# Kernel tuning notes

Measured on AMD Instinct MI355X. Metric: run time of the kernel, lower is better.

## Reference

```python
import jax, jax.numpy as jnp
import numpy as np

B, L, C, H, W = 1, 16, 16, 128, 256  # L = T_chunk = K_chunk (single chunk, causal)
DECAY = 0.1  # decay_val


def setup_inputs() -> dict:
    key = jax.random.key(0)
    k1, k2 = jax.random.split(key)
    img = jax.random.normal(k1, (B, L, C, H, W), jnp.float32)
    # flows in normalized [-1,1] grid units; keep displacements modest
    cum_flow = jax.random.normal(k2, (B, L, 2, H, W), jnp.float32) * 0.1
    t = jnp.arange(L)
    mask = (t[:, None] >= t[None, :]).astype(jnp.float32)          # causal [T,K]
    decay_dist = jnp.abs(t[:, None] - t[None, :]).astype(jnp.float32)  # [T,K]
    return {"img": img, "cum_flow": cum_flow, "mask": mask, "decay_dist": decay_dist}


def _bilinear_sample(img, gx, gy):
    # img: [B,K,C,H,W]; gx, gy: [B,K,H,W] in normalized [-1,1] coords.
    # x wraps around (periodic), y clamps -- matching the kernel's index handling.
    ix = (gx + 1.0) * (W * 0.5) - 0.5
    iy = (gy + 1.0) * (H * 0.5) - 0.5
    x0 = jnp.floor(ix)
    y0 = jnp.floor(iy)
    wx = ix - x0  # fractional weights
    wy = iy - y0
    x0i = x0.astype(jnp.int32)
    y0i = y0.astype(jnp.int32)
    x0r = jnp.mod(x0i, W)
    x1r = jnpp = jnp.mod(x0i + 1, W)
    y0c = jnp.clip(y0i, 0, H - 1)
    y1c = jnp.clip(y0i + 1, 0, H - 1)

    K = img.shape[1]
    imgf = img.reshape(B, K, C, H * W)

    def gather(yy, xx):
        idx = (yy * W + xx).reshape(B, K, 1, H * W)  # broadcast over C
        return jnp.take_along_axis(imgf, idx, axis=-1).reshape(B, K, C, H, W)

    va = gather(y0c, x0r)  # (y0, x0)
    vb = gather(y1c, x0r)  # (y1, x0)
    vc = gather(y0c, x1r)  # (y0, x1)
    vd = gather(y1c, x1r)  # (y1, x1)
    wx_ = wx[:, :, None]   # [B,K,1,H,W]
    wy_ = wy[:, :, None]
    return (va * (1.0 - wx_) * (1.0 - wy_) + vb * (1.0 - wx_) * wy_
            + vc * wx_ * (1.0 - wy_) + vd * wx_ * wy_)


def reference(img, cum_flow, mask, decay_dist):
    # base grid (align_corners=False style pixel centers)
    base_x = (jnp.arange(W, dtype=jnp.float32) * (2.0 / W) - 1.0 + 1.0 / W)[None, None, :]  # [1,1,W]
    base_y = (jnp.arange(H, dtype=jnp.float32) * (2.0 / H) - 1.0 + 1.0 / H)[None, :, None]  # [1,H,1]

    weights = mask * jnp.exp(-DECAY * decay_dist)  # [T,K] decay-weighted causal mask
    fx = cum_flow[:, :, 0]  # [B,L,H,W]
    fy = cum_flow[:, :, 1]

    def step(carry, inp):
        ft_x, ft_y, w_row = inp  # ft_*: [B,H,W]; w_row: [K]
        gx = base_x[None] + (ft_x[:, None] - fx)  # [B,K,H,W]
        gy = base_y[None] + (ft_y[:, None] - fy)
        gx = jnp.mod(gx + 1.0, 2.0) - 1.0          # wrap x into [-1,1)
        sampled = _bilinear_sample(img, gx, gy)    # [B,K,C,H,W]
        out_t = jnp.einsum('k,bkchw->bchw', w_row, sampled)
        return carry, out_t

    xs = (jnp.moveaxis(fx, 1, 0), jnp.moveaxis(fy, 1, 0), weights)  # over t
    _, outs = jax.lax.scan(step, 0.0, xs)          # [T,B,C,H,W]
    return jnp.moveaxis(outs, 0, 1)                # [B,T,C,H,W]
```

## Files before the change

### kernel.cpp

```cpp
#include <hip/hip_runtime.h>

constexpr int Lc = 16;
constexpr int Cc = 16;
constexpr int Hc = 128;
constexpr int Wc = 256;
constexpr float DECAYc = 0.1f;
constexpr int HWc = Hc * Wc;

__device__ inline unsigned short f2bf(float f) {
    unsigned int u = __float_as_uint(f);
    u += 0x7fffu + ((u >> 16) & 1u);
    return (unsigned short)(u >> 16);
}
__device__ inline float2 bf2f2(unsigned int u) {
    return make_float2(__uint_as_float(u << 16),
                       __uint_as_float(u & 0xffff0000u));
}

constexpr int topbit(unsigned m) { int r = 0; while (m >>= 1) ++r; return r; }

__global__ __launch_bounds__(256) void transpose_cvt_bf16(
    const float* __restrict__ img, unsigned short* __restrict__ imgTb)
{
    const int tid = threadIdx.x;
    const int h2 = tid & 1;
    const int wq = tid >> 1;
    const int kf  = blockIdx.x >> 5;
    const int px0 = (blockIdx.x & 31) * 1024;
    const float* __restrict__ srcb = img + (size_t)kf * Cc * HWc + (size_t)(8 * h2) * HWc;
#pragma unroll
    for (int rr = 0; rr < 8; ++rr) {
        const int px = px0 + rr * 128 + wq;
        float v[8];
#pragma unroll
        for (int c = 0; c < 8; ++c) v[c] = srcb[c * HWc + px];
        uint4 o;
        o.x = (unsigned int)f2bf(v[0]) | ((unsigned int)f2bf(v[1]) << 16);
        o.y = (unsigned int)f2bf(v[2]) | ((unsigned int)f2bf(v[3]) << 16);
        o.z = (unsigned int)f2bf(v[4]) | ((unsigned int)f2bf(v[5]) << 16);
        o.w = (unsigned int)f2bf(v[6]) | ((unsigned int)f2bf(v[7]) << 16);
        *(uint4*)(imgTb + ((size_t)kf * HWc + px) * Cc + 8 * h2) = o;
    }
}

template <unsigned MASK, int TLO, int THI>
__device__ __forceinline__ void do_chunk16(
    int k, const unsigned short* __restrict__ bk, int half,
    const float* sx1, const float* sy1, float fxk, float fyk,
    const float* __restrict__ wtab, float (*acc)[8])
{
    constexpr int NT = THI - TLO + 1;
    int   offs[NT][4];
    float wts [NT][4];
    uint4 ld  [NT][4];

#pragma unroll
    for (int t = TLO; t <= THI; ++t) {
        if (!((MASK >> t) & 1u)) continue;
        if (t > k) {
            const int j = t - TLO;
            const float wkt = wtab[t * Lc + k];
            const float ix = (sx1[t] - fxk) * (Wc * 0.5f) - 0.5f;
            const float iy = (sy1[t] - fyk) * (Hc * 0.5f) - 0.5f;
            const float x0f = floorf(ix);
            const float y0f = floorf(iy);
            const float wx = ix - x0f;
            const float wy = iy - y0f;
            const int x0 = (int)x0f;
            const int y0 = (int)y0f;
            const int x0r = x0 & (Wc - 1);
            const int x1r = (x0 + 1) & (Wc - 1);
            const int y0c = min(max(y0, 0), Hc - 1);
            const int y1c = min(max(y0 + 1, 0), Hc - 1);
            const float wb = wkt * wy;
            const float wa = wkt - wb;
            const float omx = 1.0f - wx;
            wts[j][0] = wa * omx;
            wts[j][1] = wa * wx;
            wts[j][2] = wb * omx;
            wts[j][3] = wb * wx;
            offs[j][0] = y0c * Wc + x0r;
            offs[j][1] = y0c * Wc + x1r;
            offs[j][2] = y1c * Wc + x0r;
            offs[j][3] = y1c * Wc + x1r;
        }
    }
#pragma unroll
    for (int t = TLO; t <= THI; ++t) {
        if (!((MASK >> t) & 1u)) continue;
        if (t > k) {
            const int j = t - TLO;
#pragma unroll
            for (int n = 0; n < 4; ++n)
                ld[j][n] = ((const uint4*)(bk + (size_t)offs[j][n] * Cc))[half];
        }
    }
#pragma unroll
    for (int t = TLO; t <= THI; ++t) {
        if (!((MASK >> t) & 1u)) continue;
        if (t > k) {
            const int j = t - TLO;
#pragma unroll
            for (int n = 0; n < 4; ++n) {
                const float a = wts[j][n];
                const float2 f01 = bf2f2(ld[j][n].x);
                const float2 f23 = bf2f2(ld[j][n].y);
                const float2 f45 = bf2f2(ld[j][n].z);
                const float2 f67 = bf2f2(ld[j][n].w);
                acc[t][0] += a * f01.x;
                acc[t][1] += a * f01.y;
                acc[t][2] += a * f23.x;
                acc[t][3] += a * f23.y;
                acc[t][4] += a * f45.x;
                acc[t][5] += a * f45.y;
                acc[t][6] += a * f67.x;
                acc[t][7] += a * f67.y;
            }
        }
    }
}

template <unsigned MASK>
__device__ __forceinline__ void run_quarter(
    const unsigned short* __restrict__ imgTb,
    const float* __restrict__ cum_flow,
    const float* __restrict__ img,
    float* __restrict__ out,
    const float* wtab,
    int half, int pix, float base_x, float base_y)
{
    constexpr unsigned LOOPM = MASK & ~1u;

    float sx1[Lc], sy1[Lc];
#pragma unroll
    for (int t = 0; t < Lc; ++t) {
        if (!((LOOPM >> t) & 1u)) continue;
        sx1[t] = base_x + cum_flow[(t * 2 + 0) * HWc + pix] + 1.0f;
        sy1[t] = base_y + cum_flow[(t * 2 + 1) * HWc + pix] + 1.0f;
    }

    float acc[Lc][8];
#pragma unroll
    for (int t = 0; t < Lc; ++t) {
        if (!((MASK >> t) & 1u)) continue;
#pragma unroll
        for (int c = 0; c < 8; ++c) acc[t][c] = 0.f;
    }

    constexpr int KMAX = topbit(MASK);
    for (int k = 0; k < KMAX; ++k) {
        const float fxk = cum_flow[(k * 2 + 0) * HWc + pix];
        const float fyk = cum_flow[(k * 2 + 1) * HWc + pix];
        const unsigned short* __restrict__ bk = imgTb + (size_t)k * HWc * Cc;
        do_chunk16<LOOPM, 1, 7>(k, bk, half, sx1, sy1, fxk, fyk, wtab, acc);
        do_chunk16<LOOPM, 8, 15>(k, bk, half, sx1, sy1, fxk, fyk, wtab, acc);
    }

#pragma unroll
    for (int t = 0; t < Lc; ++t) {
        if (!((MASK >> t) & 1u)) continue;
        const float* __restrict__ ip = img + ((size_t)t * Cc + 8 * half) * HWc + pix;
        float* __restrict__ op = out + ((size_t)t * Cc + 8 * half) * HWc + pix;
#pragma unroll
        for (int c = 0; c < 8; ++c)
            op[c * HWc] = acc[t][c] + ip[c * HWc];
    }
}

__global__ __launch_bounds__(256, 4) void gridsample_bf16_h16(
    const unsigned short* __restrict__ imgTb,
    const float* __restrict__ cum_flow,
    const float* __restrict__ mask,
    const float* __restrict__ decay,
    const float* __restrict__ img,
    float* __restrict__ out)
{
    __shared__ float wtab[Lc * Lc];
    const int tid = threadIdx.x;
    if (tid < Lc * Lc)
        wtab[tid] = mask[tid] * __expf(-DECAYc * decay[tid]);
    __syncthreads();

    const int half = tid & 1;
    const int px32 = (tid >> 1) & 31;
    const int wv   = tid >> 6;
    const int b    = blockIdx.x;
    const int band = b & 7;
    const int sub  = b >> 3;
    const int h = band * 16 + (sub >> 3);
    const int w = (sub & 7) * 32 + px32;
    const int pix = h * Wc + w;

    const float base_x = w * (2.0f / Wc) - 1.0f + 1.0f / Wc;
    const float base_y = h * (2.0f / Hc) - 1.0f + 1.0f / Hc;

    switch (wv) {
        case 0:  run_quarter<0x8124u>(imgTb, cum_flow, img, out, wtab, half, pix, base_x, base_y); break;
        case 1:  run_quarter<0x4242u>(imgTb, cum_flow, img, out, wtab, half, pix, base_x, base_y); break;
        case 2:  run_quarter<0x2418u>(imgTb, cum_flow, img, out, wtab, half, pix, base_x, base_y); break;
        default: run_quarter<0x1881u>(imgTb, cum_flow, img, out, wtab, half, pix, base_x, base_y); break;
    }
}

__global__ __launch_bounds__(256) void gridsample_warp_acc(
    const float* __restrict__ img, const float* __restrict__ cum_flow,
    const float* __restrict__ mask, const float* __restrict__ decay,
    float* __restrict__ out)
{
    const int w = threadIdx.x, h = blockIdx.x, t = blockIdx.y;
    const int pix = h * Wc + w;
    const float base_x = w * (2.0f / Wc) - 1.0f + 1.0f / Wc;
    const float base_y = h * (2.0f / Hc) - 1.0f + 1.0f / Hc;
    const float fxt = cum_flow[(t * 2 + 0) * HWc + pix];
    const float fyt = cum_flow[(t * 2 + 1) * HWc + pix];
    float acc[Cc];
#pragma unroll
    for (int c = 0; c < Cc; ++c) acc[c] = 0.0f;
    for (int k = 0; k <= t; ++k) {
        const float wkt = mask[t * Lc + k] * __expf(-DECAYc * decay[t * Lc + k]);
        const float fxk = cum_flow[(k * 2 + 0) * HWc + pix];
        const float fyk = cum_flow[(k * 2 + 1) * HWc + pix];
        float gx = base_x + (fxt - fxk);
        const float gy = base_y + (fyt - fyk);
        float m = gx + 1.0f;
        m -= 2.0f * floorf(m * 0.5f);
        gx = m - 1.0f;
        const float ix = (gx + 1.0f) * (Wc * 0.5f) - 0.5f;
        const float iy = (gy + 1.0f) * (Hc * 0.5f) - 0.5f;
        const float x0f = floorf(ix), y0f = floorf(iy);
        const float wx = ix - x0f, wy = iy - y0f;
        const int x0 = (int)x0f, y0 = (int)y0f;
        const int x0r = x0 & (Wc - 1), x1r = (x0 + 1) & (Wc - 1);
        const int y0c = min(max(y0, 0), Hc - 1), y1c = min(max(y0 + 1, 0), Hc - 1);
        const float a00 = wkt * (1.0f - wx) * (1.0f - wy);
        const float a01 = wkt * (1.0f - wx) * wy;
        const float a10 = wkt * wx * (1.0f - wy);
        const float a11 = wkt * wx * wy;
        const int o00 = y0c * Wc + x0r, o01 = y1c * Wc + x0r;
        const int o10 = y0c * Wc + x1r, o11 = y1c * Wc + x1r;
        const float* __restrict__ ik = img + (size_t)k * Cc * HWc;
#pragma unroll
        for (int c = 0; c < Cc; ++c) {
            const float* __restrict__ p = ik + c * HWc;
            acc[c] += p[o00] * a00 + p[o01] * a01 + p[o10] * a10 + p[o11] * a11;
        }
    }
    float* __restrict__ op = out + (size_t)t * Cc * HWc + pix;
#pragma unroll
    for (int c = 0; c < Cc; ++c) op[c * HWc] = acc[c];
}

extern "C" void kernel_launch(void* const* d_in, const int* in_sizes, int n_in,
                              void* d_out, int out_size, void* d_ws, size_t ws_size,
                              hipStream_t stream) {
    const float* img      = (const float*)d_in[0];
    const float* cum_flow = (const float*)d_in[1];
    const float* mask     = (const float*)d_in[2];
    const float* decay    = (const float*)d_in[3];
    float* out = (float*)d_out;

    const size_t needed = (size_t)Lc * HWc * Cc * sizeof(unsigned short);
    if (ws_size >= needed) {
        unsigned short* imgTb = (unsigned short*)d_ws;
        transpose_cvt_bf16<<<dim3(512), 256, 0, stream>>>(img, imgTb);
        gridsample_bf16_h16<<<dim3(1024), 256, 0, stream>>>(
            imgTb, cum_flow, mask, decay, img, out);
    } else {
        dim3 grid(Hc, Lc, 1);
        gridsample_warp_acc<<<grid, Wc, 0, stream>>>(img, cum_flow, mask, decay, out);
    }
}
```

Baseline: 162.6 us.

## Split channel halves across blocks so each wave covers 64 contiguous pixels

Before, the two 8-channel halves of a pixel sat in adjacent lanes of a wave, so each wave covered 32 pixels. Now the channel half is chosen per block (the top bit of the block index), and each wave handles 64 consecutive pixels of one half. Per-pixel flow loads and output stores become fully coalesced 64-wide accesses with no lane pairs sharing a pixel. The cost is that each bilinear gather now reads 16 bytes at a 32-byte stride, and each wave recomputes offsets and weights for twice as many distinct pixels, with cache reuse between the two halves spread across different blocks.

```diff
diff --git a/kernel.cpp b/kernel.cpp
--- a/kernel.cpp
+++ b/kernel.cpp
@@ -45,7 +45,7 @@
 
 template <unsigned MASK, int TLO, int THI>
 __device__ __forceinline__ void do_chunk16(
-    int k, const unsigned short* __restrict__ bk, int half,
+    int k, const unsigned short* __restrict__ bk,
     const float* sx1, const float* sy1, float fxk, float fyk,
     const float* __restrict__ wtab, float (*acc)[8])
 {
@@ -92,7 +92,7 @@
             const int j = t - TLO;
 #pragma unroll
             for (int n = 0; n < 4; ++n)
-                ld[j][n] = ((const uint4*)(bk + (size_t)offs[j][n] * Cc))[half];
+                ld[j][n] = *(const uint4*)(bk + (size_t)offs[j][n] * Cc);
         }
     }
 #pragma unroll
@@ -122,12 +122,12 @@
 
 template <unsigned MASK>
 __device__ __forceinline__ void run_quarter(
-    const unsigned short* __restrict__ imgTb,
+    const unsigned short* __restrict__ imgTbH,
     const float* __restrict__ cum_flow,
-    const float* __restrict__ img,
-    float* __restrict__ out,
+    const float* __restrict__ imgH,
+    float* __restrict__ outH,
     const float* wtab,
-    int half, int pix, float base_x, float base_y)
+    int pix, float base_x, float base_y)
 {
     constexpr unsigned LOOPM = MASK & ~1u;
 
@@ -151,23 +151,23 @@
     for (int k = 0; k < KMAX; ++k) {
         const float fxk = cum_flow[(k * 2 + 0) * HWc + pix];
         const float fyk = cum_flow[(k * 2 + 1) * HWc + pix];
-        const unsigned short* __restrict__ bk = imgTb + (size_t)k * HWc * Cc;
-        do_chunk16<LOOPM, 1, 7>(k, bk, half, sx1, sy1, fxk, fyk, wtab, acc);
-        do_chunk16<LOOPM, 8, 15>(k, bk, half, sx1, sy1, fxk, fyk, wtab, acc);
+        const unsigned short* __restrict__ bk = imgTbH + (size_t)k * HWc * Cc;
+        do_chunk16<LOOPM, 1, 7>(k, bk, sx1, sy1, fxk, fyk, wtab, acc);
+        do_chunk16<LOOPM, 8, 15>(k, bk, sx1, sy1, fxk, fyk, wtab, acc);
     }
 
 #pragma unroll
     for (int t = 0; t < Lc; ++t) {
         if (!((MASK >> t) & 1u)) continue;
-        const float* __restrict__ ip = img + ((size_t)t * Cc + 8 * half) * HWc + pix;
-        float* __restrict__ op = out + ((size_t)t * Cc + 8 * half) * HWc + pix;
+        const float* __restrict__ ip = imgH + (size_t)t * Cc * HWc + pix;
+        float* __restrict__ op = outH + (size_t)t * Cc * HWc + pix;
 #pragma unroll
         for (int c = 0; c < 8; ++c)
             op[c * HWc] = acc[t][c] + ip[c * HWc];
     }
 }
 
-__global__ __launch_bounds__(256, 4) void gridsample_bf16_h16(
+__global__ __launch_bounds__(256, 4) void gridsample_bf16_q64(
     const unsigned short* __restrict__ imgTb,
     const float* __restrict__ cum_flow,
     const float* __restrict__ mask,
@@ -181,24 +181,29 @@
         wtab[tid] = mask[tid] * __expf(-DECAYc * decay[tid]);
     __syncthreads();
 
-    const int half = tid & 1;
-    const int px32 = (tid >> 1) & 31;
+    const int lane = tid & 63;
     const int wv   = tid >> 6;
     const int b    = blockIdx.x;
-    const int band = b & 7;
-    const int sub  = b >> 3;
-    const int h = band * 16 + (sub >> 3);
-    const int w = (sub & 7) * 32 + px32;
+    const int half = b >> 9;
+    const int pb   = b & 511;
+    const int band = pb & 7;
+    const int sub  = pb >> 3;
+    const int h = band * 16 + (sub >> 2);
+    const int w = (sub & 3) * 64 + lane;
     const int pix = h * Wc + w;
 
     const float base_x = w * (2.0f / Wc) - 1.0f + 1.0f / Wc;
     const float base_y = h * (2.0f / Hc) - 1.0f + 1.0f / Hc;
 
+    const unsigned short* __restrict__ imgTbH = imgTb + 8 * half;
+    const float* __restrict__ imgH = img + (size_t)(8 * half) * HWc;
+    float* __restrict__ outH = out + (size_t)(8 * half) * HWc;
+
     switch (wv) {
-        case 0:  run_quarter<0x8124u>(imgTb, cum_flow, img, out, wtab, half, pix, base_x, base_y); break;
-        case 1:  run_quarter<0x4242u>(imgTb, cum_flow, img, out, wtab, half, pix, base_x, base_y); break;
-        case 2:  run_quarter<0x2418u>(imgTb, cum_flow, img, out, wtab, half, pix, base_x, base_y); break;
-        default: run_quarter<0x1881u>(imgTb, cum_flow, img, out, wtab, half, pix, base_x, base_y); break;
+        case 0:  run_quarter<0x8124u>(imgTbH, cum_flow, imgH, outH, wtab, pix, base_x, base_y); break;
+        case 1:  run_quarter<0x4242u>(imgTbH, cum_flow, imgH, outH, wtab, pix, base_x, base_y); break;
+        case 2:  run_quarter<0x2418u>(imgTbH, cum_flow, imgH, outH, wtab, pix, base_x, base_y); break;
+        default: run_quarter<0x1881u>(imgTbH, cum_flow, imgH, outH, wtab, pix, base_x, base_y); break;
     }
 }
 
@@ -263,7 +268,7 @@
     if (ws_size >= needed) {
         unsigned short* imgTb = (unsigned short*)d_ws;
         transpose_cvt_bf16<<<dim3(512), 256, 0, stream>>>(img, imgTb);
-        gridsample_bf16_h16<<<dim3(1024), 256, 0, stream>>>(
+        gridsample_bf16_q64<<<dim3(1024), 256, 0, stream>>>(
             imgTb, cum_flow, mask, decay, img, out);
     } else {
         dim3 grid(Hc, Lc, 1);
```

New measurement: 218.3 us. 1.34x slower.
